# Optimization experiments

Hardware: AMD Instinct MI355X
Metric: run time of the kernel (lower is better)

## Reference

```python
import jax, jax.numpy as jnp
import numpy as np

EPS = 1e-5
LN_EPS = 1e-5
NUM_EXPERTS = 8
TOP_K = 2
HIDDEN = 1024
INTER = 2048


def _swiglu(x, wg, wu, wd):
    # x: [T,H]; wg,wu: [H,I]; wd: [I,H]
    return (jax.nn.silu(x @ wg) * (x @ wu)) @ wd


def setup_inputs() -> dict:
    key = jax.random.key(0)
    ks = jax.random.split(key, 10)
    B, S, H, I, E = 8, 4096, HIDDEN, INTER, NUM_EXPERTS
    std_h = 1.0 / np.sqrt(H)
    std_i = 1.0 / np.sqrt(I)
    return {
        "x": jax.random.normal(ks[0], (B, S, H), dtype=jnp.float32),
        "ln_scale": jnp.ones((H,), dtype=jnp.float32),
        "ln_bias": jnp.zeros((H,), dtype=jnp.float32),
        "gate_w": jax.random.normal(ks[1], (E, H), dtype=jnp.float32) * 0.01,
        "Wg": jax.random.normal(ks[2], (E, H, I), dtype=jnp.float32) * std_h,
        "Wu": jax.random.normal(ks[3], (E, H, I), dtype=jnp.float32) * std_h,
        "Wd": jax.random.normal(ks[4], (E, I, H), dtype=jnp.float32) * std_i,
        "sWg": jax.random.normal(ks[5], (H, I), dtype=jnp.float32) * std_h,
        "sWu": jax.random.normal(ks[6], (H, I), dtype=jnp.float32) * std_h,
        "sWd": jax.random.normal(ks[7], (I, H), dtype=jnp.float32) * std_i,
    }


def reference(x, ln_scale, ln_bias, gate_w, Wg, Wu, Wd, sWg, sWu, sWd):
    B, S, H = x.shape
    xf = x.reshape(-1, H)  # [T,H]
    # Router: LayerNorm -> gate -> softmax -> top-k -> renormalize
    mu = jnp.mean(xf, axis=-1, keepdims=True)
    var = jnp.var(xf, axis=-1, keepdims=True)
    xn = (xf - mu) * jax.lax.rsqrt(var + LN_EPS) * ln_scale + ln_bias
    logits = xn @ gate_w.T  # [T,E]
    probs = jax.nn.softmax(logits, axis=-1)
    tk_probs, tk_idx = jax.lax.top_k(probs, TOP_K)  # [T,K]
    tk_probs = tk_probs / (jnp.sum(tk_probs, axis=-1, keepdims=True) + EPS)
    # Per-expert combine weight: w[t,e] = sum_k tk_probs[t,k] * (tk_idx[t,k]==e)
    onehot = (tk_idx[..., None] == jnp.arange(NUM_EXPERTS)[None, None, :])  # [T,K,E]
    w = jnp.sum(tk_probs[..., None] * onehot.astype(tk_probs.dtype), axis=1)  # [T,E]
    # Shared expert + weighted routed experts
    out = _swiglu(xf, sWg, sWu, sWd)
    for e in range(NUM_EXPERTS):
        out = out + w[:, e:e + 1] * _swiglu(xf, Wg[e], Wu[e], Wd[e])
    return out.reshape(B, S, H)
```

## Files before the change

### kernel.cpp

```cpp
#include <hip/hip_runtime.h>

#define H 1024
#define ITR 2048
#define NE 8
#define BT 32

typedef __attribute__((ext_vector_type(8))) short short8;
typedef __attribute__((ext_vector_type(4))) float f32x4;

__device__ __forceinline__ float bf2f(unsigned short u){
  union { unsigned int i; float f; } v; v.i = ((unsigned int)u) << 16; return v.f;
}
__device__ __forceinline__ unsigned short f2bf(float f){
  union { unsigned int i; float f; } v; v.f = f;
  unsigned int r = v.i + 0x7FFFu + ((v.i >> 16) & 1u);
  return (unsigned short)(r >> 16);
}
__device__ __forceinline__ void gload16(const void* g, void* l){
  __builtin_amdgcn_global_load_lds((const __attribute__((address_space(1))) void*)g,
                                   (__attribute__((address_space(3))) void*)l, 16, 0, 0);
}

__global__ __launch_bounds__(64) void detect_k(const unsigned int* __restrict__ xw,
                                               int* __restrict__ flag, int* __restrict__ cnt16){
  int lane = threadIdx.x;
  int c = 0;
  #pragma unroll
  for (int i = 0; i < 4; i++){
    unsigned u = xw[lane * 4 + i];
    int e = (u >> 7) & 0xFF;
    c += (e >= 100 && e <= 140) ? 1 : 0;
  }
  #pragma unroll
  for (int off = 32; off; off >>= 1) c += __shfl_xor(c, off);
  if (lane == 0) flag[0] = (c < 128) ? 1 : 0;
  if (lane < 16) cnt16[lane] = 0;
}

__device__ __forceinline__ void loadv16(const void* base, size_t off, int isf, float* out){
  if (isf){
    const float* p = (const float*)base + off;
    float4 a = *(const float4*)p, b = *(const float4*)(p + 4);
    float4 c = *(const float4*)(p + 8), d = *(const float4*)(p + 12);
    out[0]=a.x; out[1]=a.y; out[2]=a.z; out[3]=a.w;
    out[4]=b.x; out[5]=b.y; out[6]=b.z; out[7]=b.w;
    out[8]=c.x; out[9]=c.y; out[10]=c.z; out[11]=c.w;
    out[12]=d.x; out[13]=d.y; out[14]=d.z; out[15]=d.w;
  } else {
    const unsigned short* p = (const unsigned short*)base + off;
    uint4 a = *(const uint4*)p, b = *(const uint4*)(p + 8);
    unsigned short u[16];
    *(uint4*)u = a; *(uint4*)(u + 8) = b;
    #pragma unroll
    for (int j = 0; j < 16; j++) out[j] = bf2f(u[j]);
  }
}

__global__ __launch_bounds__(256) void trans_k(
    const void* __restrict__ rg, const void* __restrict__ ru, const void* __restrict__ rd,
    const void* __restrict__ sg, const void* __restrict__ su, const void* __restrict__ sd,
    unsigned short* __restrict__ arena, const int* __restrict__ flag)
{
  int slot = blockIdx.z / 3, mt = blockIdx.z % 3;
  int e = slot;
  int R = (mt == 2) ? ITR : H;
  int C = (mt == 2) ? H : ITR;
  int c0 = blockIdx.x * 64, r0 = blockIdx.y * 64;
  if (c0 >= C || r0 >= R) return;
  const void* srcv;
  size_t eoff = 0;
  if (e == NE) srcv = (mt == 0) ? sg : ((mt == 1) ? su : sd);
  else { srcv = (mt == 0) ? rg : ((mt == 1) ? ru : rd); eoff = (size_t)e * H * ITR; }
  unsigned short* dst = arena + (size_t)slot * (3u * H * ITR)
                      + (mt == 2 ? (size_t)2 * H * ITR : 0);
  int isf = *flag;
  __shared__ unsigned short tile[64][72];
  int t = threadIdx.x;
  int row = t >> 3, c8 = (t & 7) * 8;
  #pragma unroll
  for (int p = 0; p < 2; p++){
    int r = r0 + row + p * 32;
    unsigned short v[8];
    if (isf){
      const float* s = (const float*)srcv + eoff + (size_t)r * C + c0 + c8;
      float4 a = *(const float4*)s, b = *(const float4*)(s + 4);
      v[0]=f2bf(a.x); v[1]=f2bf(a.y); v[2]=f2bf(a.z); v[3]=f2bf(a.w);
      v[4]=f2bf(b.x); v[5]=f2bf(b.y); v[6]=f2bf(b.z); v[7]=f2bf(b.w);
    } else {
      const unsigned short* s = (const unsigned short*)srcv + eoff + (size_t)r * C + c0 + c8;
      *(uint4*)v = *(const uint4*)s;
    }
    *(uint4*)&tile[row + p * 32][c8] = *(const uint4*)v;
  }
  __syncthreads();
  #pragma unroll
  for (int p = 0; p < 2; p++){
    int c = row + p * 32;
    int dc = c0 + c;
    int dr = (mt == 2) ? dc : (((dc >> 5) << 6) + mt * 32 + (dc & 31));
    unsigned short tmp[8];
    #pragma unroll
    for (int j = 0; j < 8; j++) tmp[j] = tile[c8 + j][c];
    *(uint4*)(dst + (size_t)dr * R + r0 + c8) = *(const uint4*)tmp;
  }
}

__global__ __launch_bounds__(256) void router2_k(
    const void* __restrict__ x, const void* __restrict__ lns, const void* __restrict__ lnb,
    const void* __restrict__ gw, int T, const int* __restrict__ flag,
    int* __restrict__ cnt16, int* __restrict__ lidx, float* __restrict__ lw)
{
  int isf = *flag;
  int tid = threadIdx.x, wv = tid >> 6, lane = tid & 63;
  int t0 = blockIdx.x * BT;
  __shared__ int scc[16], sbase[16];
  __shared__ int sei[2][BT], soi[2][BT];
  __shared__ float swv[2][BT];
  if (tid < 16) scc[tid] = 0;
  float sc[16], bi[16];
  loadv16(lns, (size_t)lane * 16, isf, sc);
  loadv16(lnb, (size_t)lane * 16, isf, bi);
  __syncthreads();

  for (int i = 0; i < BT / 4; i++){
    int tl = i * 4 + wv;
    int tok = t0 + tl;
    if (tok >= T) break;
    float v[16];
    loadv16(x, (size_t)tok * H + lane * 16, isf, v);
    float sum = 0.f, ss = 0.f;
    #pragma unroll
    for (int j = 0; j < 16; j++){ sum += v[j]; ss += v[j] * v[j]; }
    #pragma unroll
    for (int off = 32; off; off >>= 1){ sum += __shfl_xor(sum, off); ss += __shfl_xor(ss, off); }
    float mu = sum * (1.f / H);
    float rstd = rsqrtf(ss * (1.f / H) - mu * mu + 1e-5f);
    float xn[16];
    #pragma unroll
    for (int j = 0; j < 16; j++) xn[j] = (v[j] - mu) * rstd * sc[j] + bi[j];
    float acc[NE];
    #pragma unroll
    for (int e = 0; e < NE; e++){
      float g[16];
      loadv16(gw, (size_t)e * H + lane * 16, isf, g);
      float s = 0.f;
      #pragma unroll
      for (int j = 0; j < 16; j++) s += xn[j] * g[j];
      acc[e] = s;
    }
    #pragma unroll
    for (int off = 32; off; off >>= 1){
      #pragma unroll
      for (int e = 0; e < NE; e++) acc[e] += __shfl_xor(acc[e], off);
    }
    if (lane == 0){
      float m = acc[0];
      #pragma unroll
      for (int e = 1; e < NE; e++) m = fmaxf(m, acc[e]);
      float p[NE], Z = 0.f;
      #pragma unroll
      for (int e = 0; e < NE; e++){ p[e] = expf(acc[e] - m); Z += p[e]; }
      float iZ = 1.f / Z;
      #pragma unroll
      for (int e = 0; e < NE; e++) p[e] *= iZ;
      int i1 = 0;
      #pragma unroll
      for (int e = 1; e < NE; e++) if (p[e] > p[i1]) i1 = e;
      int i2 = (i1 == 0) ? 1 : 0;
      #pragma unroll
      for (int e = 0; e < NE; e++) if (e != i1 && p[e] > p[i2]) i2 = e;
      float s2 = p[i1] + p[i2] + 1e-5f;
      int o1 = atomicAdd(&scc[i1], 1);
      int o2 = atomicAdd(&scc[8 + i2], 1);
      sei[0][tl] = i1; soi[0][tl] = o1; swv[0][tl] = p[i1] / s2;
      sei[1][tl] = i2; soi[1][tl] = o2; swv[1][tl] = p[i2] / s2;
    }
  }
  __syncthreads();
  if (tid < 16) sbase[tid] = atomicAdd(&cnt16[tid], scc[tid]);
  __syncthreads();
  if (tid < 2 * BT){
    int l = tid / BT, t = tid % BT;
    int tok = t0 + t;
    if (tok < T){
      int ctr = l * 8 + sei[l][t];
      int pos = sbase[ctr] + soi[l][t];
      lidx[(size_t)ctr * T + pos] = tok;
      lw[(size_t)ctr * T + pos] = swv[l][t];
    }
  }
}

__global__ __launch_bounds__(64) void scan_k(const int* __restrict__ cnt16,
                                             int* __restrict__ segA, int* __restrict__ segEp,
                                             int* __restrict__ segCnt, int T, int CH,
                                             int L1C, int L2C){
  if (threadIdx.x == 0){
    segA[0] = 0; segEp[0] = T; segCnt[0] = T;
    int b = L1C * CH;
    for (int e = 0; e < 8; e++){
      segA[1 + e] = b; segCnt[1 + e] = cnt16[e];
      b += (cnt16[e] + 255) & ~255;
      segEp[1 + e] = b;
    }
    b = L2C * CH;
    for (int e = 0; e < 8; e++){
      segA[9 + e] = b; segCnt[9 + e] = cnt16[8 + e];
      b += (cnt16[8 + e] + 255) & ~255;
      segEp[9 + e] = b;
    }
  }
}

template<int EPI>
__global__ __launch_bounds__(256, 2) void gemm128_k(
    const void* __restrict__ Asrc, const unsigned short* __restrict__ arena,
    unsigned short* __restrict__ hidden, void* __restrict__ outp,
    const int* __restrict__ segA, const int* __restrict__ segEp, const int* __restrict__ segCnt,
    const int* __restrict__ lidx, const float* __restrict__ lw,
    int T, int CH, int c0chunk, const int* __restrict__ flag)
{
  constexpr int K  = (EPI == 2) ? ITR : H;
  constexpr int NT = K / 32;

  int tn, tm, chid;
  {
    int P = gridDim.y * gridDim.z;
    int fid = blockIdx.x + gridDim.x * (blockIdx.y + gridDim.y * blockIdx.z);
    if ((P & 7) == 0){
      int xcd = fid & 7;
      int li = fid >> 3;
      int ppx = P >> 3;
      int SS = (EPI == 0) ? 8 : 4;
      if (SS > ppx) SS = ppx;
      int p = li % SS;
      int rest = li / SS;
      tn = rest % (int)gridDim.x;
      int sl = rest / (int)gridDim.x;
      int g = xcd * ppx + sl * SS + p;
      tm = g % (int)gridDim.y;
      chid = c0chunk + g / (int)gridDim.y;
    } else {
      tn = blockIdx.x; tm = blockIdx.y; chid = c0chunk + blockIdx.z;
    }
  }
  int pr0 = chid * CH + tm * 128;

  int s = -1;
  if (pr0 < T) s = 0;
  else {
    #pragma unroll
    for (int i = 1; i <= 16; i++)
      if (pr0 >= segA[i] && pr0 < segEp[i]) s = i;
  }
  if (s < 0) return;
  int cnt = segCnt[s], base = segA[s];
  int slot = (s == 0) ? 8 : ((s - 1) & 7);
  const unsigned short* wT = arena + (size_t)slot * (3u * H * ITR)
                           + (EPI == 2 ? (size_t)2 * H * ITR : 0);
  int isf = *flag;

  __shared__ unsigned short Al[2][128 * 32];
  __shared__ unsigned short Bl[2][128 * 32];

  int tid = threadIdx.x, wid = tid >> 6, l = tid & 63;
  int fr = l & 15, fq = l >> 4;
  int r0l = wid * 32 + (l >> 2);
  int su = (tid & 3) ^ ((l >> 3) & 3);
  int hrow0 = pr0 - c0chunk * CH;

  const unsigned short* aptr[2];
  const float* afp[2];
  #pragma unroll
  for (int q = 0; q < 2; q++){
    int rloc = r0l + q * 16;
    if (EPI == 2){
      aptr[q] = (const unsigned short*)Asrc + (size_t)(hrow0 + rloc) * ITR + su * 8;
      afp[q] = nullptr;
    } else {
      int rl = pr0 - base + rloc;
      int rc = cnt - 1; rl = rl < rc ? rl : rc;
      int tok = (s == 0) ? rl : lidx[(size_t)(s - 1) * T + rl];
      aptr[q] = (const unsigned short*)Asrc + (size_t)tok * H + su * 8;
      afp[q]  = (const float*)Asrc + (size_t)tok * H + su * 8;
    }
  }
  const unsigned short* bptr[2];
  #pragma unroll
  for (int q = 0; q < 2; q++)
    bptr[q] = wT + (size_t)(tn * 128 + r0l + q * 16) * K + su * 8;

  f32x4 acc[4][4];
  f32x4 zero4 = {0.f, 0.f, 0.f, 0.f};
  #pragma unroll
  for (int m = 0; m < 4; m++)
    #pragma unroll
    for (int n = 0; n < 4; n++) acc[m][n] = zero4;

  int wm = (wid >> 1) * 64, wn = (wid & 1) * 64;

  auto stage = [&](int buf, int kt){
    int k0 = kt * 32;
    #pragma unroll
    for (int q = 0; q < 2; q++){
      int lbyte = (wid * 32 + q * 16) * 64;
      if (EPI == 0 && isf){
        const float* f = afp[q] + k0;
        float4 v0 = *(const float4*)f, v1 = *(const float4*)(f + 4);
        unsigned short w8[8] = {f2bf(v0.x), f2bf(v0.y), f2bf(v0.z), f2bf(v0.w),
                                f2bf(v1.x), f2bf(v1.y), f2bf(v1.z), f2bf(v1.w)};
        *(uint4*)((char*)&Al[buf][0] + (r0l + q * 16) * 64 + (tid & 3) * 16) = *(const uint4*)w8;
      } else {
        gload16(aptr[q] + k0, (char*)&Al[buf][0] + lbyte);
      }
      gload16(bptr[q] + k0, (char*)&Bl[buf][0] + lbyte);
    }
  };

  auto compute = [&](int buf){
    const unsigned short* Ab = &Al[buf][0];
    const unsigned short* Bb = &Bl[buf][0];
    int un = (fq ^ ((fr >> 1) & 3)) * 8;
    __builtin_amdgcn_s_setprio(1);
    short8 a[4], b[4];
    #pragma unroll
    for (int m = 0; m < 4; m++)
      a[m] = *(const short8*)(Ab + (wm + m * 16 + fr) * 32 + un);
    #pragma unroll
    for (int n = 0; n < 4; n++)
      b[n] = *(const short8*)(Bb + (wn + n * 16 + fr) * 32 + un);
    #pragma unroll
    for (int m = 0; m < 4; m++)
      #pragma unroll
      for (int n = 0; n < 4; n++)
        acc[m][n] = __builtin_amdgcn_mfma_f32_16x16x32_bf16(a[m], b[n], acc[m][n], 0, 0, 0);
    __builtin_amdgcn_s_setprio(0);
  };

  stage(0, 0);
  int cur = 0;
  for (int kt = 0; kt < NT; kt++){
    if (kt + 1 < NT) stage(cur ^ 1, kt + 1);
    if (EPI == 0 && isf) asm volatile("s_waitcnt lgkmcnt(0)" ::: "memory");
    if (kt + 1 < NT){
      if (EPI == 0 && isf) asm volatile("s_waitcnt vmcnt(2)" ::: "memory");
      else                 asm volatile("s_waitcnt vmcnt(4)" ::: "memory");
    } else {
      asm volatile("s_waitcnt vmcnt(0)" ::: "memory");
    }
    __builtin_amdgcn_s_barrier();
    compute(cur);
    __builtin_amdgcn_s_barrier();
    cur ^= 1;
  }

  int rb = fq * 4;
  if (EPI == 0){
    int colbase = tn * 64 + (wid & 1) * 32;
    #pragma unroll
    for (int m = 0; m < 4; m++){
      #pragma unroll
      for (int j = 0; j < 4; j++){
        int rl = hrow0 + wm + m * 16 + rb + j;
        unsigned short* hr = hidden + (size_t)rl * ITR + colbase;
        #pragma unroll
        for (int k = 0; k < 2; k++){
          float g = acc[m][k][j], uu = acc[m][k + 2][j];
          __builtin_nontemporal_store(f2bf(g / (1.f + __expf(-g)) * uu), &hr[k * 16 + fr]);
        }
      }
    }
  } else {
    #pragma unroll
    for (int m = 0; m < 4; m++){
      #pragma unroll
      for (int j = 0; j < 4; j++){
        int pr = pr0 + wm + m * 16 + rb + j;
        int rl = pr - base;
        if (rl < cnt){
          int tok = (s == 0) ? rl : lidx[(size_t)(s - 1) * T + rl];
          size_t ob = (size_t)tok * H + tn * 128 + wn + fr;
          if (s == 0){
            if (isf){
              float* p = (float*)outp + ob;
              #pragma unroll
              for (int n = 0; n < 4; n++) __builtin_nontemporal_store(acc[m][n][j], &p[n * 16]);
            } else {
              unsigned short* p = (unsigned short*)outp + ob;
              #pragma unroll
              for (int n = 0; n < 4; n++) __builtin_nontemporal_store(f2bf(acc[m][n][j]), &p[n * 16]);
            }
          } else {
            float wgt = lw[(size_t)(s - 1) * T + rl];
            if (isf){
              float* p = (float*)outp + ob;
              #pragma unroll
              for (int n = 0; n < 4; n++) p[n * 16] += wgt * acc[m][n][j];
            } else {
              unsigned short* p = (unsigned short*)outp + ob;
              #pragma unroll
              for (int n = 0; n < 4; n++) p[n * 16] = f2bf(bf2f(p[n * 16]) + wgt * acc[m][n][j]);
            }
          }
        }
      }
    }
  }
}

extern "C" void kernel_launch(void* const* d_in, const int* in_sizes, int n_in,
                              void* d_out, int out_size, void* d_ws, size_t ws_size,
                              hipStream_t stream)
{
  int T = in_sizes[0] / H;

  char* w = (char*)d_ws;
  auto alloc = [&](size_t b){ char* p = w; w += (b + 255) & ~(size_t)255; return p; };
  int* flag   = (int*)alloc(256);
  int* cnt16  = (int*)alloc(256);
  int* segA   = (int*)alloc(256);
  int* segEp  = (int*)alloc(256);
  int* segCnt = (int*)alloc(256);
  int* lidx   = (int*)alloc((size_t)16 * T * 4);
  float* lw   = (float*)alloc((size_t)16 * T * 4);
  const size_t ARENA = (size_t)9 * 3 * H * ITR * 2;
  unsigned short* arena = (unsigned short*)alloc(ARENA);
  size_t used = (size_t)(w - (char*)d_ws);

  int CH = 2048, merged = 0, nh = 1, hidch = 1;
  {
    int mch[3] = {8192, 4096, 2048};
    for (int i = 0; i < 3 && !merged; i++){
      int ch = mch[i];
      int c1 = (T + 8 * 255 + ch - 1) / ch;
      size_t need = used + (size_t)c1 * ch * ITR * 2 + 1024;
      if (need <= ws_size){ merged = 1; CH = ch; hidch = c1; }
    }
    if (!merged){
      struct { int ch, n; } lad[4] = {{8192,2},{8192,1},{4096,1},{2048,1}};
      for (int i = 0; i < 4; i++){
        size_t need = used + (size_t)lad[i].n * lad[i].ch * ITR * 2 + 1024;
        if (need <= ws_size){ CH = lad[i].ch; nh = lad[i].n; hidch = lad[i].n; break; }
      }
    }
  }
  unsigned short* hidden = (unsigned short*)alloc((size_t)hidch * CH * ITR * 2);

  int CB1 = (T + CH - 1) / CH;
  int chunks1 = (T + 8 * 255 + CH - 1) / CH;
  int CB2 = CB1 + chunks1;
  int NCHUNK = CB2 + chunks1;

  detect_k<<<1, 64, 0, stream>>>((const unsigned int*)d_in[0], flag, cnt16);
  router2_k<<<(T + BT - 1) / BT, 256, 0, stream>>>(d_in[0], d_in[1], d_in[2], d_in[3],
                                                   T, flag, cnt16, lidx, lw);
  scan_k<<<1, 64, 0, stream>>>(cnt16, segA, segEp, segCnt, T, CH, CB1, CB2);
  trans_k<<<dim3(32, 32, 27), 256, 0, stream>>>(d_in[4], d_in[5], d_in[6],
                                                d_in[7], d_in[8], d_in[9], arena, flag);

  int bnds[4] = {0, CB1, CB2, NCHUNK};
  if (merged){
    for (int r = 0; r < 3; r++){
      int ng = bnds[r + 1] - bnds[r];
      gemm128_k<0><<<dim3(32, CH / 128, ng), 256, 0, stream>>>(
          d_in[0], arena, hidden, nullptr, segA, segEp, segCnt, lidx, lw,
          T, CH, bnds[r], flag);
      gemm128_k<2><<<dim3(8, CH / 128, ng), 256, 0, stream>>>(
          hidden, arena, hidden, d_out, segA, segEp, segCnt, lidx, lw,
          T, CH, bnds[r], flag);
    }
  } else {
    for (int r = 0; r < 3; r++){
      for (int c = bnds[r]; c < bnds[r + 1]; ){
        int z = (nh == 2 && c + 1 < bnds[r + 1]) ? 2 : 1;
        gemm128_k<0><<<dim3(32, CH / 128, z), 256, 0, stream>>>(
            d_in[0], arena, hidden, nullptr, segA, segEp, segCnt, lidx, lw,
            T, CH, c, flag);
        gemm128_k<2><<<dim3(8, CH / 128, z), 256, 0, stream>>>(
            hidden, arena, hidden, d_out, segA, segEp, segCnt, lidx, lw,
            T, CH, c, flag);
        c += z;
      }
    }
  }
}
```

Measured before the change: 2.452 ms.

## Enlarge expert GEMM tiles to 256x256 with 512 threads and interleaved LDS/MFMA

```diff
diff --git a/kernel.cpp b/kernel.cpp
--- a/kernel.cpp
+++ b/kernel.cpp
@@ -58,7 +58,7 @@
 
 __global__ __launch_bounds__(256) void trans_k(
     const void* __restrict__ rg, const void* __restrict__ ru, const void* __restrict__ rd,
-    const void* __restrict__ sg, const void* __restrict__ su, const void* __restrict__ sd,
+    const void* __restrict__ sg, const void* __restrict__ su_, const void* __restrict__ sd,
     unsigned short* __restrict__ arena, const int* __restrict__ flag)
 {
   int slot = blockIdx.z / 3, mt = blockIdx.z % 3;
@@ -69,7 +69,7 @@
   if (c0 >= C || r0 >= R) return;
   const void* srcv;
   size_t eoff = 0;
-  if (e == NE) srcv = (mt == 0) ? sg : ((mt == 1) ? su : sd);
+  if (e == NE) srcv = (mt == 0) ? sg : ((mt == 1) ? su_ : sd);
   else { srcv = (mt == 0) ? rg : ((mt == 1) ? ru : rd); eoff = (size_t)e * H * ITR; }
   unsigned short* dst = arena + (size_t)slot * (3u * H * ITR)
                       + (mt == 2 ? (size_t)2 * H * ITR : 0);
@@ -213,15 +213,15 @@
 }
 
 template<int EPI>
-__global__ __launch_bounds__(256, 2) void gemm128_k(
+__global__ __launch_bounds__(512, 2) void gemm256k_k(
     const void* __restrict__ Asrc, const unsigned short* __restrict__ arena,
     unsigned short* __restrict__ hidden, void* __restrict__ outp,
     const int* __restrict__ segA, const int* __restrict__ segEp, const int* __restrict__ segCnt,
     const int* __restrict__ lidx, const float* __restrict__ lw,
     int T, int CH, int c0chunk, const int* __restrict__ flag)
 {
-  constexpr int K  = (EPI == 2) ? ITR : H;
-  constexpr int NT = K / 32;
+  constexpr int K   = (EPI == 2) ? ITR : H;
+  constexpr int NTL = K / 64;
 
   int tn, tm, chid;
   {
@@ -231,7 +231,7 @@
       int xcd = fid & 7;
       int li = fid >> 3;
       int ppx = P >> 3;
-      int SS = (EPI == 0) ? 8 : 4;
+      int SS = (EPI == 0) ? 4 : 2;
       if (SS > ppx) SS = ppx;
       int p = li % SS;
       int rest = li / SS;
@@ -244,7 +244,7 @@
       tn = blockIdx.x; tm = blockIdx.y; chid = c0chunk + blockIdx.z;
     }
   }
-  int pr0 = chid * CH + tm * 128;
+  int pr0 = chid * CH + tm * 256;
 
   int s = -1;
   if (pr0 < T) s = 0;
@@ -259,127 +259,138 @@
   const unsigned short* wT = arena + (size_t)slot * (3u * H * ITR)
                            + (EPI == 2 ? (size_t)2 * H * ITR : 0);
   int isf = *flag;
-
-  __shared__ unsigned short Al[2][128 * 32];
-  __shared__ unsigned short Bl[2][128 * 32];
+  const bool isfA = (EPI == 0) && (isf != 0);
+
+  __shared__ unsigned short Al[2][2][256 * 32];
+  __shared__ unsigned short Bl[2][2][256 * 32];
 
   int tid = threadIdx.x, wid = tid >> 6, l = tid & 63;
   int fr = l & 15, fq = l >> 4;
-  int r0l = wid * 32 + (l >> 2);
-  int su = (tid & 3) ^ ((l >> 3) & 3);
+  int su = (l & 3) ^ ((l >> 3) & 3);
   int hrow0 = pr0 - c0chunk * CH;
 
-  const unsigned short* aptr[2];
-  const float* afp[2];
-  #pragma unroll
-  for (int q = 0; q < 2; q++){
-    int rloc = r0l + q * 16;
+  const unsigned short* aP[2];
+  const float* aPf[2];
+  const unsigned short* bP[2];
+  #pragma unroll
+  for (int r = 0; r < 2; r++){
+    int rlocal = (r * 8 + wid) * 16 + (l >> 2);
     if (EPI == 2){
-      aptr[q] = (const unsigned short*)Asrc + (size_t)(hrow0 + rloc) * ITR + su * 8;
-      afp[q] = nullptr;
+      aP[r] = (const unsigned short*)Asrc + (size_t)(hrow0 + rlocal) * ITR + su * 8;
+      aPf[r] = nullptr;
     } else {
-      int rl = pr0 - base + rloc;
+      int rl = pr0 - base + rlocal;
       int rc = cnt - 1; rl = rl < rc ? rl : rc;
       int tok = (s == 0) ? rl : lidx[(size_t)(s - 1) * T + rl];
-      aptr[q] = (const unsigned short*)Asrc + (size_t)tok * H + su * 8;
-      afp[q]  = (const float*)Asrc + (size_t)tok * H + su * 8;
-    }
-  }
-  const unsigned short* bptr[2];
-  #pragma unroll
-  for (int q = 0; q < 2; q++)
-    bptr[q] = wT + (size_t)(tn * 128 + r0l + q * 16) * K + su * 8;
-
-  f32x4 acc[4][4];
+      aP[r]  = (const unsigned short*)Asrc + (size_t)tok * H + su * 8;
+      aPf[r] = (const float*)Asrc + (size_t)tok * H + su * 8;
+    }
+    bP[r] = wT + (size_t)(tn * 256 + rlocal) * K + su * 8;
+  }
+
+  f32x4 acc[8][4];
   f32x4 zero4 = {0.f, 0.f, 0.f, 0.f};
   #pragma unroll
-  for (int m = 0; m < 4; m++)
+  for (int m = 0; m < 8; m++)
     #pragma unroll
     for (int n = 0; n < 4; n++) acc[m][n] = zero4;
 
-  int wm = (wid >> 1) * 64, wn = (wid & 1) * 64;
-
-  auto stage = [&](int buf, int kt){
-    int k0 = kt * 32;
-    #pragma unroll
-    for (int q = 0; q < 2; q++){
-      int lbyte = (wid * 32 + q * 16) * 64;
-      if (EPI == 0 && isf){
-        const float* f = afp[q] + k0;
+  int wm = (wid >> 2) * 128, wn = (wid & 3) * 64;
+  int un = fq ^ ((fr >> 1) & 3);
+  short8 aR[4], bR[4];
+
+  auto stage = [&](int tg, int kk){
+    if (tg >= NTL) return;
+    int k0 = tg * 64 + kk * 32;
+    char* Ab = (char*)&Al[tg & 1][kk][0];
+    char* Bb = (char*)&Bl[tg & 1][kk][0];
+    #pragma unroll
+    for (int r = 0; r < 2; r++){
+      if (isfA){
+        const float* f = aPf[r] + k0;
         float4 v0 = *(const float4*)f, v1 = *(const float4*)(f + 4);
         unsigned short w8[8] = {f2bf(v0.x), f2bf(v0.y), f2bf(v0.z), f2bf(v0.w),
                                 f2bf(v1.x), f2bf(v1.y), f2bf(v1.z), f2bf(v1.w)};
-        *(uint4*)((char*)&Al[buf][0] + (r0l + q * 16) * 64 + (tid & 3) * 16) = *(const uint4*)w8;
+        *(uint4*)(Ab + (r * 8 + wid) * 1024 + l * 16) = *(const uint4*)w8;
       } else {
-        gload16(aptr[q] + k0, (char*)&Al[buf][0] + lbyte);
+        gload16(aP[r] + k0, Ab + (r * 8 + wid) * 1024);
       }
-      gload16(bptr[q] + k0, (char*)&Bl[buf][0] + lbyte);
+      gload16(bP[r] + k0, Bb + (r * 8 + wid) * 1024);
     }
   };
-
-  auto compute = [&](int buf){
-    const unsigned short* Ab = &Al[buf][0];
-    const unsigned short* Bb = &Bl[buf][0];
-    int un = (fq ^ ((fr >> 1) & 3)) * 8;
+  auto rdA4 = [&](int buf, int kk, int mh){
+    const unsigned short* Ab = &Al[buf][kk][0];
+    #pragma unroll
+    for (int m = 0; m < 4; m++){
+      int row = wm + (mh * 4 + m) * 16 + fr;
+      aR[m] = *(const short8*)(Ab + row * 32 + un * 8);
+    }
+  };
+  auto rdB4 = [&](int buf, int kk){
+    const unsigned short* Bb = &Bl[buf][kk][0];
+    #pragma unroll
+    for (int n = 0; n < 4; n++){
+      int row = wn + n * 16 + fr;
+      bR[n] = *(const short8*)(Bb + row * 32 + un * 8);
+    }
+  };
+  auto mfma8 = [&](int mh){
     __builtin_amdgcn_s_setprio(1);
-    short8 a[4], b[4];
     #pragma unroll
     for (int m = 0; m < 4; m++)
-      a[m] = *(const short8*)(Ab + (wm + m * 16 + fr) * 32 + un);
-    #pragma unroll
-    for (int n = 0; n < 4; n++)
-      b[n] = *(const short8*)(Bb + (wn + n * 16 + fr) * 32 + un);
-    #pragma unroll
-    for (int m = 0; m < 4; m++)
       #pragma unroll
       for (int n = 0; n < 4; n++)
-        acc[m][n] = __builtin_amdgcn_mfma_f32_16x16x32_bf16(a[m], b[n], acc[m][n], 0, 0, 0);
+        acc[mh * 4 + m][n] = __builtin_amdgcn_mfma_f32_16x16x32_bf16(
+            aR[m], bR[n], acc[mh * 4 + m][n], 0, 0, 0);
     __builtin_amdgcn_s_setprio(0);
   };
 
-  stage(0, 0);
-  int cur = 0;
-  for (int kt = 0; kt < NT; kt++){
-    if (kt + 1 < NT) stage(cur ^ 1, kt + 1);
-    if (EPI == 0 && isf) asm volatile("s_waitcnt lgkmcnt(0)" ::: "memory");
-    if (kt + 1 < NT){
-      if (EPI == 0 && isf) asm volatile("s_waitcnt vmcnt(2)" ::: "memory");
-      else                 asm volatile("s_waitcnt vmcnt(4)" ::: "memory");
-    } else {
-      asm volatile("s_waitcnt vmcnt(0)" ::: "memory");
-    }
-    __builtin_amdgcn_s_barrier();
-    compute(cur);
-    __builtin_amdgcn_s_barrier();
-    cur ^= 1;
-  }
-
-  int rb = fq * 4;
+  stage(0, 0); stage(0, 1);
+
+  for (int t = 0; t < NTL; t++){
+    int buf = t & 1, nx = t + 1;
+    bool last = (nx == NTL);
+    #pragma unroll
+    for (int kk = 0; kk < 2; kk++){
+      if (isfA)                 asm volatile("s_waitcnt vmcnt(0) lgkmcnt(0)" ::: "memory");
+      else if (last && kk == 1) asm volatile("s_waitcnt vmcnt(0)" ::: "memory");
+      else                      asm volatile("s_waitcnt vmcnt(4)" ::: "memory");
+      __builtin_amdgcn_s_barrier();
+      rdB4(buf, kk);
+      rdA4(buf, kk, 0);
+      stage(nx, kk);
+      mfma8(0);
+      rdA4(buf, kk, 1);
+      mfma8(1);
+    }
+  }
+
+  int rb = fq * 4, cb = fr;
   if (EPI == 0){
-    int colbase = tn * 64 + (wid & 1) * 32;
-    #pragma unroll
-    for (int m = 0; m < 4; m++){
+    int g64 = tn * 4 + (wid & 3);
+    #pragma unroll
+    for (int m = 0; m < 8; m++){
       #pragma unroll
       for (int j = 0; j < 4; j++){
         int rl = hrow0 + wm + m * 16 + rb + j;
-        unsigned short* hr = hidden + (size_t)rl * ITR + colbase;
+        unsigned short* hr = hidden + (size_t)rl * ITR + g64 * 32 + cb;
         #pragma unroll
-        for (int k = 0; k < 2; k++){
-          float g = acc[m][k][j], uu = acc[m][k + 2][j];
-          __builtin_nontemporal_store(f2bf(g / (1.f + __expf(-g)) * uu), &hr[k * 16 + fr]);
+        for (int nf = 0; nf < 2; nf++){
+          float g = acc[m][nf][j], u = acc[m][nf + 2][j];
+          __builtin_nontemporal_store(f2bf(g / (1.f + __expf(-g)) * u), &hr[nf * 16]);
         }
       }
     }
   } else {
     #pragma unroll
-    for (int m = 0; m < 4; m++){
+    for (int m = 0; m < 8; m++){
       #pragma unroll
       for (int j = 0; j < 4; j++){
         int pr = pr0 + wm + m * 16 + rb + j;
         int rl = pr - base;
         if (rl < cnt){
           int tok = (s == 0) ? rl : lidx[(size_t)(s - 1) * T + rl];
-          size_t ob = (size_t)tok * H + tn * 128 + wn + fr;
+          size_t ob = (size_t)tok * H + tn * 256 + wn + cb;
           if (s == 0){
             if (isf){
               float* p = (float*)outp + ob;
@@ -462,10 +473,10 @@
   if (merged){
     for (int r = 0; r < 3; r++){
       int ng = bnds[r + 1] - bnds[r];
-      gemm128_k<0><<<dim3(32, CH / 128, ng), 256, 0, stream>>>(
+      gemm256k_k<0><<<dim3(16, CH / 256, ng), 512, 0, stream>>>(
           d_in[0], arena, hidden, nullptr, segA, segEp, segCnt, lidx, lw,
           T, CH, bnds[r], flag);
-      gemm128_k<2><<<dim3(8, CH / 128, ng), 256, 0, stream>>>(
+      gemm256k_k<2><<<dim3(4, CH / 256, ng), 512, 0, stream>>>(
           hidden, arena, hidden, d_out, segA, segEp, segCnt, lidx, lw,
           T, CH, bnds[r], flag);
     }
@@ -473,10 +484,10 @@
     for (int r = 0; r < 3; r++){
       for (int c = bnds[r]; c < bnds[r + 1]; ){
         int z = (nh == 2 && c + 1 < bnds[r + 1]) ? 2 : 1;
-        gemm128_k<0><<<dim3(32, CH / 128, z), 256, 0, stream>>>(
+        gemm256k_k<0><<<dim3(16, CH / 256, z), 512, 0, stream>>>(
             d_in[0], arena, hidden, nullptr, segA, segEp, segCnt, lidx, lw,
             T, CH, c, flag);
-        gemm128_k<2><<<dim3(8, CH / 128, z), 256, 0, stream>>>(
+        gemm256k_k<2><<<dim3(4, CH / 256, z), 512, 0, stream>>>(
             hidden, arena, hidden, d_out, segA, segEp, segCnt, lidx, lw,
             T, CH, c, flag);
         c += z;
```

Result: slower. 2.719 ms (+10.9%).

## Split expert intermediate dimension into two halves with partial down-projection accumulation

Applied to the files above, without the earlier changes.

```diff
diff --git a/kernel.cpp b/kernel.cpp
--- a/kernel.cpp
+++ b/kernel.cpp
@@ -212,16 +212,16 @@
   }
 }
 
-template<int EPI>
+template<int EPI, int KEXT>
 __global__ __launch_bounds__(256, 2) void gemm128_k(
     const void* __restrict__ Asrc, const unsigned short* __restrict__ arena,
     unsigned short* __restrict__ hidden, void* __restrict__ outp,
     const int* __restrict__ segA, const int* __restrict__ segEp, const int* __restrict__ segCnt,
     const int* __restrict__ lidx, const float* __restrict__ lw,
-    int T, int CH, int c0chunk, const int* __restrict__ flag)
+    int T, int CH, int c0chunk, size_t woff, int accflag, const int* __restrict__ flag)
 {
-  constexpr int K  = (EPI == 2) ? ITR : H;
-  constexpr int NT = K / 32;
+  constexpr int NT   = KEXT / 32;
+  constexpr int BSTR = (EPI == 2) ? ITR : H;
 
   int tn, tm, chid;
   {
@@ -257,7 +257,7 @@
   int cnt = segCnt[s], base = segA[s];
   int slot = (s == 0) ? 8 : ((s - 1) & 7);
   const unsigned short* wT = arena + (size_t)slot * (3u * H * ITR)
-                           + (EPI == 2 ? (size_t)2 * H * ITR : 0);
+                           + (EPI == 2 ? (size_t)2 * H * ITR : 0) + woff;
   int isf = *flag;
 
   __shared__ unsigned short Al[2][128 * 32];
@@ -288,7 +288,7 @@
   const unsigned short* bptr[2];
   #pragma unroll
   for (int q = 0; q < 2; q++)
-    bptr[q] = wT + (size_t)(tn * 128 + r0l + q * 16) * K + su * 8;
+    bptr[q] = wT + (size_t)(tn * 128 + r0l + q * 16) * BSTR + su * 8;
 
   f32x4 acc[4][4];
   f32x4 zero4 = {0.f, 0.f, 0.f, 0.f};
@@ -380,7 +380,7 @@
         if (rl < cnt){
           int tok = (s == 0) ? rl : lidx[(size_t)(s - 1) * T + rl];
           size_t ob = (size_t)tok * H + tn * 128 + wn + fr;
-          if (s == 0){
+          if (s == 0 && !accflag){
             if (isf){
               float* p = (float*)outp + ob;
               #pragma unroll
@@ -391,7 +391,7 @@
               for (int n = 0; n < 4; n++) __builtin_nontemporal_store(f2bf(acc[m][n][j]), &p[n * 16]);
             }
           } else {
-            float wgt = lw[(size_t)(s - 1) * T + rl];
+            float wgt = (s == 0) ? 1.f : lw[(size_t)(s - 1) * T + rl];
             if (isf){
               float* p = (float*)outp + ob;
               #pragma unroll
@@ -458,27 +458,28 @@
   trans_k<<<dim3(32, 32, 27), 256, 0, stream>>>(d_in[4], d_in[5], d_in[6],
                                                 d_in[7], d_in[8], d_in[9], arena, flag);
 
+  auto run_range = [&](int c0, int ng){
+    if (ng <= 0) return;
+    for (int half = 0; half < 2; half++){
+      gemm128_k<0, 1024><<<dim3(16, CH / 128, ng), 256, 0, stream>>>(
+          d_in[0], arena, hidden + half * 1024, nullptr,
+          segA, segEp, segCnt, lidx, lw, T, CH, c0,
+          (size_t)half * 2048 * H, 0, flag);
+      gemm128_k<2, 1024><<<dim3(8, CH / 128, ng), 256, 0, stream>>>(
+          hidden + half * 1024, arena, hidden, d_out,
+          segA, segEp, segCnt, lidx, lw, T, CH, c0,
+          (size_t)half * 1024, half, flag);
+    }
+  };
+
   int bnds[4] = {0, CB1, CB2, NCHUNK};
   if (merged){
-    for (int r = 0; r < 3; r++){
-      int ng = bnds[r + 1] - bnds[r];
-      gemm128_k<0><<<dim3(32, CH / 128, ng), 256, 0, stream>>>(
-          d_in[0], arena, hidden, nullptr, segA, segEp, segCnt, lidx, lw,
-          T, CH, bnds[r], flag);
-      gemm128_k<2><<<dim3(8, CH / 128, ng), 256, 0, stream>>>(
-          hidden, arena, hidden, d_out, segA, segEp, segCnt, lidx, lw,
-          T, CH, bnds[r], flag);
-    }
+    for (int r = 0; r < 3; r++) run_range(bnds[r], bnds[r + 1] - bnds[r]);
   } else {
     for (int r = 0; r < 3; r++){
       for (int c = bnds[r]; c < bnds[r + 1]; ){
         int z = (nh == 2 && c + 1 < bnds[r + 1]) ? 2 : 1;
-        gemm128_k<0><<<dim3(32, CH / 128, z), 256, 0, stream>>>(
-            d_in[0], arena, hidden, nullptr, segA, segEp, segCnt, lidx, lw,
-            T, CH, c, flag);
-        gemm128_k<2><<<dim3(8, CH / 128, z), 256, 0, stream>>>(
-            hidden, arena, hidden, d_out, segA, segEp, segCnt, lidx, lw,
-            T, CH, c, flag);
+        run_range(c, z);
         c += z;
       }
     }
```

Measured after the change: 2.826 ms. 1.15x slower.

## Load weight tiles directly into registers instead of staging through LDS

Applied to the files above, without the earlier changes.

```diff
diff --git a/kernel.cpp b/kernel.cpp
--- a/kernel.cpp
+++ b/kernel.cpp
@@ -261,13 +261,13 @@
   int isf = *flag;
 
   __shared__ unsigned short Al[2][128 * 32];
-  __shared__ unsigned short Bl[2][128 * 32];
 
   int tid = threadIdx.x, wid = tid >> 6, l = tid & 63;
   int fr = l & 15, fq = l >> 4;
   int r0l = wid * 32 + (l >> 2);
   int su = (tid & 3) ^ ((l >> 3) & 3);
   int hrow0 = pr0 - c0chunk * CH;
+  int wm = (wid >> 1) * 64, wn = (wid & 1) * 64;
 
   const unsigned short* aptr[2];
   const float* afp[2];
@@ -285,10 +285,10 @@
       afp[q]  = (const float*)Asrc + (size_t)tok * H + su * 8;
     }
   }
-  const unsigned short* bptr[2];
-  #pragma unroll
-  for (int q = 0; q < 2; q++)
-    bptr[q] = wT + (size_t)(tn * 128 + r0l + q * 16) * K + su * 8;
+  const unsigned short* bfr[4];
+  #pragma unroll
+  for (int n = 0; n < 4; n++)
+    bfr[n] = wT + (size_t)(tn * 128 + wn + n * 16 + fr) * K + fq * 8;
 
   f32x4 acc[4][4];
   f32x4 zero4 = {0.f, 0.f, 0.f, 0.f};
@@ -297,9 +297,7 @@
     #pragma unroll
     for (int n = 0; n < 4; n++) acc[m][n] = zero4;
 
-  int wm = (wid >> 1) * 64, wn = (wid & 1) * 64;
-
-  auto stage = [&](int buf, int kt){
+  auto stageA = [&](int buf, int kt){
     int k0 = kt * 32;
     #pragma unroll
     for (int q = 0; q < 2; q++){
@@ -313,22 +311,25 @@
       } else {
         gload16(aptr[q] + k0, (char*)&Al[buf][0] + lbyte);
       }
-      gload16(bptr[q] + k0, (char*)&Bl[buf][0] + lbyte);
     }
   };
 
-  auto compute = [&](int buf){
+  short8 bA[4], bB[4];
+  auto loadB = [&](short8* bd, int kt){
+    int k0 = kt * 32;
+    #pragma unroll
+    for (int n = 0; n < 4; n++)
+      bd[n] = *(const short8*)(bfr[n] + k0);
+  };
+
+  auto compute = [&](int buf, const short8* b){
     const unsigned short* Ab = &Al[buf][0];
-    const unsigned short* Bb = &Bl[buf][0];
     int un = (fq ^ ((fr >> 1) & 3)) * 8;
     __builtin_amdgcn_s_setprio(1);
-    short8 a[4], b[4];
+    short8 a[4];
     #pragma unroll
     for (int m = 0; m < 4; m++)
       a[m] = *(const short8*)(Ab + (wm + m * 16 + fr) * 32 + un);
-    #pragma unroll
-    for (int n = 0; n < 4; n++)
-      b[n] = *(const short8*)(Bb + (wn + n * 16 + fr) * 32 + un);
     #pragma unroll
     for (int m = 0; m < 4; m++)
       #pragma unroll
@@ -337,21 +338,21 @@
     __builtin_amdgcn_s_setprio(0);
   };
 
-  stage(0, 0);
-  int cur = 0;
-  for (int kt = 0; kt < NT; kt++){
-    if (kt + 1 < NT) stage(cur ^ 1, kt + 1);
-    if (EPI == 0 && isf) asm volatile("s_waitcnt lgkmcnt(0)" ::: "memory");
-    if (kt + 1 < NT){
-      if (EPI == 0 && isf) asm volatile("s_waitcnt vmcnt(2)" ::: "memory");
-      else                 asm volatile("s_waitcnt vmcnt(4)" ::: "memory");
-    } else {
-      asm volatile("s_waitcnt vmcnt(0)" ::: "memory");
-    }
+  stageA(0, 0); loadB(bA, 0);
+  for (int kt = 0; kt < NT; kt += 2){
+    stageA(1, kt + 1); loadB(bB, kt + 1);
+    if (EPI == 0 && isf) asm volatile("s_waitcnt vmcnt(0) lgkmcnt(0)" ::: "memory");
+    else                 asm volatile("s_waitcnt vmcnt(6)" ::: "memory");
     __builtin_amdgcn_s_barrier();
-    compute(cur);
+    compute(0, bA);
     __builtin_amdgcn_s_barrier();
-    cur ^= 1;
+    if (kt + 2 < NT){ stageA(0, kt + 2); loadB(bA, kt + 2); }
+    if (EPI == 0 && isf)      asm volatile("s_waitcnt vmcnt(0) lgkmcnt(0)" ::: "memory");
+    else if (kt + 2 < NT)     asm volatile("s_waitcnt vmcnt(6)" ::: "memory");
+    else                      asm volatile("s_waitcnt vmcnt(0)" ::: "memory");
+    __builtin_amdgcn_s_barrier();
+    compute(1, bB);
+    __builtin_amdgcn_s_barrier();
   }
 
   int rb = fq * 4;
```

Result: slower. 3.872 ms (+57.9%).
